# Kernel optimization log

Measured on AMD Instinct MI355X. Metric: run time of the kernel, lower is better.

## Reference

```python
import jax, jax.numpy as jnp
import numpy as np

HEADS = 6
WS = 8  # window size
EPS = 1e-12  # F.normalize default eps


def _l2norm(x):
    n = jnp.linalg.norm(x, axis=-1, keepdims=True)
    return x / jnp.maximum(n, EPS)


def setup_inputs() -> dict:
    key = jax.random.key(0)
    ks = jax.random.split(key, 5)
    B, C, H, W = 4, 192, 256, 256
    x = jax.random.normal(ks[0], (B, C, H, W), dtype=jnp.float32)
    dw_w = jax.random.normal(ks[1], (C, 1, 3, 3), dtype=jnp.float32) * 0.05
    dw_b = jax.random.normal(ks[2], (C,), dtype=jnp.float32) * 0.05
    pw_w = jax.random.normal(ks[3], (3 * C, C, 1, 1), dtype=jnp.float32) * 0.05
    pw_b = jax.random.normal(ks[4], (3 * C,), dtype=jnp.float32) * 0.05
    return {"x": x, "dw_w": dw_w, "dw_b": dw_b, "pw_w": pw_w, "pw_b": pw_b}


def reference(x, dw_w, dw_b, pw_w, pw_b):
    B, C, H, W = x.shape
    dn = ('NCHW', 'OIHW', 'NCHW')
    # SeparableConv: depthwise 3x3 (pad 1) then pointwise 1x1 -> 3C channels
    y = jax.lax.conv_general_dilated(x, dw_w, (1, 1), [(1, 1), (1, 1)],
                                     dimension_numbers=dn,
                                     feature_group_count=C) + dw_b[None, :, None, None]
    qkv = jax.lax.conv_general_dilated(y, pw_w, (1, 1), [(0, 0), (0, 0)],
                                       dimension_numbers=dn) + pw_b[None, :, None, None]
    C3 = 3 * C
    qkv = qkv.transpose(0, 2, 3, 1)  # (B, H, W, 3C)  [bchw_to_blc + view]
    # window_partition -> (B*nW, WS*WS, 3C)
    qkv = qkv.reshape(B, H // WS, WS, W // WS, WS, C3)
    qkv = qkv.transpose(0, 1, 3, 2, 4, 5).reshape(-1, WS * WS, C3)
    B_, N, _ = qkv.shape
    hd = C // HEADS
    qkv = qkv.reshape(B_, N, 3, HEADS, hd).transpose(2, 0, 3, 1, 4)
    q, k, v = qkv[0], qkv[1], qkv[2]  # each (B_, heads, N, hd)
    # cosine-similarity attention: L2-normalized q, k
    attn = jnp.einsum('bhnd,bhmd->bhnm', _l2norm(q), _l2norm(k))
    attn = jax.nn.softmax(attn, axis=-1)  # attn_drop=0.0 -> identity
    o = jnp.einsum('bhnm,bhmd->bhnd', attn, v)
    o = o.transpose(0, 2, 1, 3).reshape(B_, WS, WS, C)  # (B_, ws, ws, C)
    # window_reverse -> (B, H, W, C)
    o = o.reshape(B, H // WS, W // WS, WS, WS, C)
    o = o.transpose(0, 1, 3, 2, 4, 5).reshape(B, H, W, C)
    return o.transpose(0, 3, 1, 2)  # bhwc_to_bchw
```

## Files before the change

### kernel.cpp

```cpp
#include <hip/hip_runtime.h>
#include <hip/hip_bf16.h>

typedef float f32x4 __attribute__((ext_vector_type(4)));
typedef short bf16x8 __attribute__((ext_vector_type(8)));
typedef unsigned short u16;

#define NHEADS 6
#define CIN 192
#define HD 32
#define IMG 256
#define YS_ST 200
#define QK_ST 40
#define VT_ST 72
#define P_ST  72

__device__ __forceinline__ u16 f2bf(float f) {
    __hip_bfloat16 t = __float2bfloat16(f);
    return *reinterpret_cast<u16*>(&t);
}

template<bool CHK>
__device__ __forceinline__ void dwphase(const float* __restrict__ x,
                                        const float* __restrict__ dww,
                                        const float* __restrict__ dwb,
                                        u16 (*ys)[YS_ST],
                                        int b, int r0, int c0, int lane, int wave) {
    const int pi = lane >> 3, pj = lane & 7;
    const int py = r0 + pi, px = c0 + pj;
    for (int cb = wave * 4; cb < CIN; cb += 16) {
        float acc[4];
#pragma unroll
        for (int u = 0; u < 4; ++u) acc[u] = dwb[cb + u];
#pragma unroll
        for (int di = 0; di < 3; ++di) {
            const int yy = py + di - 1;
            const bool yok = !CHK || (unsigned)yy < (unsigned)IMG;
#pragma unroll
            for (int dj = 0; dj < 3; ++dj) {
                const int xx = px + dj - 1;
                const bool ok = !CHK || (yok && (unsigned)xx < (unsigned)IMG);
#pragma unroll
                for (int u = 0; u < 4; ++u) {
                    const float* xp = x + (((size_t)(b * CIN + cb + u)) << 16);
                    const float xv = ok ? xp[yy * IMG + xx] : 0.f;
                    acc[u] += xv * dww[(cb + u) * 9 + di * 3 + dj];
                }
            }
        }
        const unsigned lo = ((unsigned)f2bf(acc[1]) << 16) | f2bf(acc[0]);
        const unsigned hi = ((unsigned)f2bf(acc[3]) << 16) | f2bf(acc[2]);
        uint2 pk; pk.x = lo; pk.y = hi;
        *(uint2*)&ys[lane][cb] = pk;
    }
}

__global__ __launch_bounds__(256, 4)
void fused_winattn_mfma(const float* __restrict__ x,
                        const float* __restrict__ dww,
                        const float* __restrict__ dwb,
                        const float* __restrict__ pww,
                        const float* __restrict__ pwb,
                        const u16* __restrict__ wbf,
                        float* __restrict__ out) {
    __shared__ __align__(16) unsigned char smem[25600];
    u16 (*ys)[YS_ST] = (u16 (*)[YS_ST])smem;
    u16 (*qs)[QK_ST] = (u16 (*)[QK_ST])smem;
    u16 (*ks)[QK_ST] = (u16 (*)[QK_ST])(smem + 5120);
    u16 (*vt)[VT_ST] = (u16 (*)[VT_ST])(smem + 10240);
    u16 (*ps)[P_ST]  = (u16 (*)[P_ST]) (smem + 14848);

    const int bid = blockIdx.x;
    const int wb  = (bid & 7) * 512 + (bid >> 3);
    const int b   = wb >> 10;
    const int wy  = (wb >> 5) & 31;
    const int wx  = wb & 31;
    const int r0 = wy << 3, c0 = wx << 3;
    const int tid  = threadIdx.x;
    const int lane = tid & 63;
    const int wave = __builtin_amdgcn_readfirstlane(tid >> 6);
    const int l15 = lane & 15;
    const int l4  = lane >> 4;

    if ((unsigned)(wy - 1) < 30u && (unsigned)(wx - 1) < 30u)
        dwphase<false>(x, dww, dwb, ys, b, r0, c0, lane, wave);
    else
        dwphase<true>(x, dww, dwb, ys, b, r0, c0, lane, wave);
    __syncthreads();

    const int wr = wave >> 1, wc = wave & 1;
    bf16x8 afr[2][6];
#pragma unroll
    for (int rt = 0; rt < 2; ++rt) {
        const u16* ab = &ys[wr * 32 + rt * 16 + l15][l4 * 8];
#pragma unroll
        for (int kt = 0; kt < 6; ++kt)
            afr[rt][kt] = *(const bf16x8*)(ab + kt * 32);
    }
    __syncthreads();

    const int m0 = wave * 16;

    for (int h = 0; h < NHEADS; ++h) {
        const int qkbase = (wc ? CIN : 0) + h * HD;
        f32x4 acc[2][2];
#pragma unroll
        for (int ct = 0; ct < 2; ++ct) {
            const int ocrow = qkbase + ct * 16 + l15;
            const float bias = pwb[ocrow];
            acc[ct][0] = (f32x4){bias, bias, bias, bias};
            acc[ct][1] = acc[ct][0];
            bf16x8 bfr[6];
            if (wbf) {
                const u16* wp = wbf + (size_t)ocrow * CIN + l4 * 8;
#pragma unroll
                for (int kt = 0; kt < 6; ++kt) bfr[kt] = *(const bf16x8*)(wp + kt * 32);
            } else {
                const float* wp = pww + (size_t)ocrow * CIN + l4 * 8;
#pragma unroll
                for (int kt = 0; kt < 6; ++kt) {
                    union { u16 u[8]; bf16x8 v; } cv;
#pragma unroll
                    for (int i = 0; i < 8; ++i) cv.u[i] = f2bf(wp[kt * 32 + i]);
                    bfr[kt] = cv.v;
                }
            }
#pragma unroll
            for (int kt = 0; kt < 6; ++kt) {
                acc[ct][0] = __builtin_amdgcn_mfma_f32_16x16x32_bf16(afr[0][kt], bfr[kt], acc[ct][0], 0, 0, 0);
                acc[ct][1] = __builtin_amdgcn_mfma_f32_16x16x32_bf16(afr[1][kt], bfr[kt], acc[ct][1], 0, 0, 0);
            }
        }
#pragma unroll
        for (int rt = 0; rt < 2; ++rt) {
            f32x4 s;
#pragma unroll
            for (int i = 0; i < 4; ++i)
                s[i] = acc[0][rt][i] * acc[0][rt][i] + acc[1][rt][i] * acc[1][rt][i];
#pragma unroll
            for (int off = 1; off < 16; off <<= 1) {
#pragma unroll
                for (int i = 0; i < 4; ++i) s[i] += __shfl_xor(s[i], off);
            }
#pragma unroll
            for (int i = 0; i < 4; ++i) {
                const float inv = 1.f / fmaxf(sqrtf(s[i]), 1e-12f);
                acc[0][rt][i] *= inv;
                acc[1][rt][i] *= inv;
            }
            const int pxr = wr * 32 + rt * 16 + l4 * 4;
            u16 (*dst)[QK_ST] = wc ? ks : qs;
#pragma unroll
            for (int ct = 0; ct < 2; ++ct)
#pragma unroll
                for (int i = 0; i < 4; ++i)
                    dst[pxr + i][ct * 16 + l15] = f2bf(acc[ct][rt][i]);
        }
        {
            const int ocrow = 2 * CIN + h * HD + wc * 16 + l15;
            const float bias = pwb[ocrow];
            f32x4 av0 = (f32x4){bias, bias, bias, bias};
            f32x4 av1 = av0;
            bf16x8 bfr[6];
            if (wbf) {
                const u16* wp = wbf + (size_t)ocrow * CIN + l4 * 8;
#pragma unroll
                for (int kt = 0; kt < 6; ++kt) bfr[kt] = *(const bf16x8*)(wp + kt * 32);
            } else {
                const float* wp = pww + (size_t)ocrow * CIN + l4 * 8;
#pragma unroll
                for (int kt = 0; kt < 6; ++kt) {
                    union { u16 u[8]; bf16x8 v; } cv;
#pragma unroll
                    for (int i = 0; i < 8; ++i) cv.u[i] = f2bf(wp[kt * 32 + i]);
                    bfr[kt] = cv.v;
                }
            }
#pragma unroll
            for (int kt = 0; kt < 6; ++kt) {
                av0 = __builtin_amdgcn_mfma_f32_16x16x32_bf16(afr[0][kt], bfr[kt], av0, 0, 0, 0);
                av1 = __builtin_amdgcn_mfma_f32_16x16x32_bf16(afr[1][kt], bfr[kt], av1, 0, 0, 0);
            }
#pragma unroll
            for (int rt = 0; rt < 2; ++rt) {
                const f32x4 a = rt ? av1 : av0;
                const int pxr = wr * 32 + rt * 16 + l4 * 4;
                const unsigned lo = ((unsigned)f2bf(a[1]) << 16) | f2bf(a[0]);
                const unsigned hi = ((unsigned)f2bf(a[3]) << 16) | f2bf(a[2]);
                uint2 pk; pk.x = lo; pk.y = hi;
                *(uint2*)&vt[wc * 16 + l15][pxr] = pk;
            }
        }
        __syncthreads();

        const bf16x8 aq = *(const bf16x8*)&qs[m0 + l15][l4 * 8];
        f32x4 sc[4];
#pragma unroll
        for (int ct = 0; ct < 4; ++ct) {
            f32x4 z = {0.f, 0.f, 0.f, 0.f};
            const bf16x8 bk = *(const bf16x8*)&ks[ct * 16 + l15][l4 * 8];
            sc[ct] = __builtin_amdgcn_mfma_f32_16x16x32_bf16(aq, bk, z, 0, 0, 0);
        }
#pragma unroll
        for (int i = 0; i < 4; ++i) {
            float mx = fmaxf(fmaxf(sc[0][i], sc[1][i]), fmaxf(sc[2][i], sc[3][i]));
#pragma unroll
            for (int off = 1; off < 16; off <<= 1) mx = fmaxf(mx, __shfl_xor(mx, off));
            const float e0 = __expf(sc[0][i] - mx), e1 = __expf(sc[1][i] - mx);
            const float e2 = __expf(sc[2][i] - mx), e3 = __expf(sc[3][i] - mx);
            float s = e0 + e1 + e2 + e3;
#pragma unroll
            for (int off = 1; off < 16; off <<= 1) s += __shfl_xor(s, off);
            const float r = 1.f / s;
            sc[0][i] = e0 * r; sc[1][i] = e1 * r; sc[2][i] = e2 * r; sc[3][i] = e3 * r;
        }
#pragma unroll
        for (int ct = 0; ct < 4; ++ct)
#pragma unroll
            for (int i = 0; i < 4; ++i)
                ps[m0 + l4 * 4 + i][ct * 16 + l15] = f2bf(sc[ct][i]);

        const bf16x8 ap0 = *(const bf16x8*)&ps[m0 + l15][l4 * 8];
        const bf16x8 ap1 = *(const bf16x8*)&ps[m0 + l15][32 + l4 * 8];
#pragma unroll
        for (int nt = 0; nt < 2; ++nt) {
            f32x4 oa = {0.f, 0.f, 0.f, 0.f};
            const bf16x8 bv0 = *(const bf16x8*)&vt[nt * 16 + l15][l4 * 8];
            const bf16x8 bv1 = *(const bf16x8*)&vt[nt * 16 + l15][32 + l4 * 8];
            oa = __builtin_amdgcn_mfma_f32_16x16x32_bf16(ap0, bv0, oa, 0, 0, 0);
            oa = __builtin_amdgcn_mfma_f32_16x16x32_bf16(ap1, bv1, oa, 0, 0, 0);
            const int dim = h * HD + nt * 16 + l15;
            const int pxr = m0 + l4 * 4;
            const int py = r0 + (pxr >> 3), pxc = c0 + (pxr & 7);
            float* op = out + (((size_t)(b * CIN + dim)) << 16) + py * IMG + pxc;
            *(f32x4*)op = oa;
        }
        __syncthreads();
    }
}

__global__ void cvt_w(const float* __restrict__ w, u16* __restrict__ o, int n) {
    const int i = blockIdx.x * 256 + threadIdx.x;
    if (i < n) o[i] = f2bf(w[i]);
}

extern "C" void kernel_launch(void* const* d_in, const int* in_sizes, int n_in,
                              void* d_out, int out_size, void* d_ws, size_t ws_size,
                              hipStream_t stream) {
    const float* x   = (const float*)d_in[0];
    const float* dww = (const float*)d_in[1];
    const float* dwb = (const float*)d_in[2];
    const float* pww = (const float*)d_in[3];
    const float* pwb = (const float*)d_in[4];
    float* out = (float*)d_out;

    const int nw = 3 * CIN * CIN;
    u16* wbf = nullptr;
    if (ws_size >= (size_t)nw * sizeof(u16)) {
        wbf = (u16*)d_ws;
        hipLaunchKernelGGL(cvt_w, dim3(nw / 256), dim3(256), 0, stream, pww, wbf, nw);
    }
    hipLaunchKernelGGL(fused_winattn_mfma, dim3(4 * 32 * 32), dim3(256), 0, stream,
                       x, dww, dwb, pww, pwb, wbf, out);
}
```

Baseline: 371.4 us.

## Prefetch next-head pointwise weights, keep ys in LDS, transpose QK^T softmax

Each head's pointwise weight fragments and biases are now loaded into registers one head ahead, so their global-load latency overlaps with the current head's work. The ys tile moves to its own LDS region with a padded stride and its A fragments are re-read from LDS every head rather than held in registers, which also drops one barrier. The score MFMA is transposed (K as A, Q as B) so each softmax row sits within a lane and needs only two cross-lane shuffles per reduction, and probabilities are written to LDS as packed 64-bit stores. LDS use roughly doubles and the occupancy hint drops from 4 to 3 blocks, trading occupancy for fewer registers spent on ys and more latency hiding.

Measured after the change: 382.0 us. +2.8%, slower.

```diff
diff --git a/kernel.cpp b/kernel.cpp
--- a/kernel.cpp
+++ b/kernel.cpp
@@ -9,7 +9,7 @@
 #define CIN 192
 #define HD 32
 #define IMG 256
-#define YS_ST 200
+#define YS_ST 208
 #define QK_ST 40
 #define VT_ST 72
 #define P_ST  72
@@ -54,7 +54,7 @@
     }
 }
 
-__global__ __launch_bounds__(256, 4)
+__global__ __launch_bounds__(256, 3)
 void fused_winattn_mfma(const float* __restrict__ x,
                         const float* __restrict__ dww,
                         const float* __restrict__ dwb,
@@ -62,12 +62,12 @@
                         const float* __restrict__ pwb,
                         const u16* __restrict__ wbf,
                         float* __restrict__ out) {
-    __shared__ __align__(16) unsigned char smem[25600];
+    __shared__ __align__(16) unsigned char smem[50688];
     u16 (*ys)[YS_ST] = (u16 (*)[YS_ST])smem;
-    u16 (*qs)[QK_ST] = (u16 (*)[QK_ST])smem;
-    u16 (*ks)[QK_ST] = (u16 (*)[QK_ST])(smem + 5120);
-    u16 (*vt)[VT_ST] = (u16 (*)[VT_ST])(smem + 10240);
-    u16 (*ps)[P_ST]  = (u16 (*)[P_ST]) (smem + 14848);
+    u16 (*qs)[QK_ST] = (u16 (*)[QK_ST])(smem + 26624);
+    u16 (*ks)[QK_ST] = (u16 (*)[QK_ST])(smem + 31744);
+    u16 (*vt)[VT_ST] = (u16 (*)[VT_ST])(smem + 36864);
+    u16 (*ps)[P_ST]  = (u16 (*)[P_ST]) (smem + 41472);
 
     const int bid = blockIdx.x;
     const int wb  = (bid & 7) * 512 + (bid >> 3);
@@ -80,6 +80,36 @@
     const int wave = __builtin_amdgcn_readfirstlane(tid >> 6);
     const int l15 = lane & 15;
     const int l4  = lane >> 4;
+    const int wr = wave >> 1, wc = wave & 1;
+    const int m0 = wave * 16;
+
+    bf16x8 wf[3][6];
+    float biasr[3];
+    auto ldfrag = [&](int ocrow, int kt) -> bf16x8 {
+        if (wbf) {
+            return *(const bf16x8*)(wbf + (size_t)ocrow * CIN + kt * 32 + l4 * 8);
+        } else {
+            union { u16 u[8]; bf16x8 v; } cv;
+            const float* wp = pww + (size_t)ocrow * CIN + kt * 32 + l4 * 8;
+#pragma unroll
+            for (int i = 0; i < 8; ++i) cv.u[i] = f2bf(wp[i]);
+            return cv.v;
+        }
+    };
+    auto loadw = [&](int h) {
+        const int rq0 = (wc ? CIN : 0) + h * HD + l15;
+        const int rq1 = rq0 + 16;
+        const int rv  = 2 * CIN + h * HD + wc * 16 + l15;
+#pragma unroll
+        for (int kt = 0; kt < 6; ++kt) {
+            wf[0][kt] = ldfrag(rq0, kt);
+            wf[1][kt] = ldfrag(rq1, kt);
+            wf[2][kt] = ldfrag(rv, kt);
+        }
+        biasr[0] = pwb[rq0]; biasr[1] = pwb[rq1]; biasr[2] = pwb[rv];
+    };
+
+    loadw(0);
 
     if ((unsigned)(wy - 1) < 30u && (unsigned)(wx - 1) < 30u)
         dwphase<false>(x, dww, dwb, ys, b, r0, c0, lane, wave);
@@ -87,55 +117,36 @@
         dwphase<true>(x, dww, dwb, ys, b, r0, c0, lane, wave);
     __syncthreads();
 
-    const int wr = wave >> 1, wc = wave & 1;
-    bf16x8 afr[2][6];
-#pragma unroll
-    for (int rt = 0; rt < 2; ++rt) {
-        const u16* ab = &ys[wr * 32 + rt * 16 + l15][l4 * 8];
-#pragma unroll
-        for (int kt = 0; kt < 6; ++kt)
-            afr[rt][kt] = *(const bf16x8*)(ab + kt * 32);
-    }
-    __syncthreads();
-
-    const int m0 = wave * 16;
-
     for (int h = 0; h < NHEADS; ++h) {
-        const int qkbase = (wc ? CIN : 0) + h * HD;
-        f32x4 acc[2][2];
+        f32x4 accq[2][2];
+        f32x4 accv[2];
 #pragma unroll
         for (int ct = 0; ct < 2; ++ct) {
-            const int ocrow = qkbase + ct * 16 + l15;
-            const float bias = pwb[ocrow];
-            acc[ct][0] = (f32x4){bias, bias, bias, bias};
-            acc[ct][1] = acc[ct][0];
-            bf16x8 bfr[6];
-            if (wbf) {
-                const u16* wp = wbf + (size_t)ocrow * CIN + l4 * 8;
-#pragma unroll
-                for (int kt = 0; kt < 6; ++kt) bfr[kt] = *(const bf16x8*)(wp + kt * 32);
-            } else {
-                const float* wp = pww + (size_t)ocrow * CIN + l4 * 8;
-#pragma unroll
-                for (int kt = 0; kt < 6; ++kt) {
-                    union { u16 u[8]; bf16x8 v; } cv;
-#pragma unroll
-                    for (int i = 0; i < 8; ++i) cv.u[i] = f2bf(wp[kt * 32 + i]);
-                    bfr[kt] = cv.v;
-                }
-            }
-#pragma unroll
-            for (int kt = 0; kt < 6; ++kt) {
-                acc[ct][0] = __builtin_amdgcn_mfma_f32_16x16x32_bf16(afr[0][kt], bfr[kt], acc[ct][0], 0, 0, 0);
-                acc[ct][1] = __builtin_amdgcn_mfma_f32_16x16x32_bf16(afr[1][kt], bfr[kt], acc[ct][1], 0, 0, 0);
-            }
-        }
+            const float bsc = biasr[ct];
+            accq[ct][0] = (f32x4){bsc, bsc, bsc, bsc};
+            accq[ct][1] = accq[ct][0];
+        }
+        accv[0] = (f32x4){biasr[2], biasr[2], biasr[2], biasr[2]};
+        accv[1] = accv[0];
+#pragma unroll
+        for (int kt = 0; kt < 6; ++kt) {
+            const bf16x8 a0 = *(const bf16x8*)&ys[wr * 32 + l15][kt * 32 + l4 * 8];
+            const bf16x8 a1 = *(const bf16x8*)&ys[wr * 32 + 16 + l15][kt * 32 + l4 * 8];
+            accq[0][0] = __builtin_amdgcn_mfma_f32_16x16x32_bf16(a0, wf[0][kt], accq[0][0], 0, 0, 0);
+            accq[0][1] = __builtin_amdgcn_mfma_f32_16x16x32_bf16(a1, wf[0][kt], accq[0][1], 0, 0, 0);
+            accq[1][0] = __builtin_amdgcn_mfma_f32_16x16x32_bf16(a0, wf[1][kt], accq[1][0], 0, 0, 0);
+            accq[1][1] = __builtin_amdgcn_mfma_f32_16x16x32_bf16(a1, wf[1][kt], accq[1][1], 0, 0, 0);
+            accv[0]    = __builtin_amdgcn_mfma_f32_16x16x32_bf16(a0, wf[2][kt], accv[0], 0, 0, 0);
+            accv[1]    = __builtin_amdgcn_mfma_f32_16x16x32_bf16(a1, wf[2][kt], accv[1], 0, 0, 0);
+        }
+        if (h < NHEADS - 1) loadw(h + 1);
+
 #pragma unroll
         for (int rt = 0; rt < 2; ++rt) {
             f32x4 s;
 #pragma unroll
             for (int i = 0; i < 4; ++i)
-                s[i] = acc[0][rt][i] * acc[0][rt][i] + acc[1][rt][i] * acc[1][rt][i];
+                s[i] = accq[0][rt][i] * accq[0][rt][i] + accq[1][rt][i] * accq[1][rt][i];
 #pragma unroll
             for (int off = 1; off < 16; off <<= 1) {
 #pragma unroll
@@ -144,8 +155,8 @@
 #pragma unroll
             for (int i = 0; i < 4; ++i) {
                 const float inv = 1.f / fmaxf(sqrtf(s[i]), 1e-12f);
-                acc[0][rt][i] *= inv;
-                acc[1][rt][i] *= inv;
+                accq[0][rt][i] *= inv;
+                accq[1][rt][i] *= inv;
             }
             const int pxr = wr * 32 + rt * 16 + l4 * 4;
             u16 (*dst)[QK_ST] = wc ? ks : qs;
@@ -153,71 +164,52 @@
             for (int ct = 0; ct < 2; ++ct)
 #pragma unroll
                 for (int i = 0; i < 4; ++i)
-                    dst[pxr + i][ct * 16 + l15] = f2bf(acc[ct][rt][i]);
-        }
-        {
-            const int ocrow = 2 * CIN + h * HD + wc * 16 + l15;
-            const float bias = pwb[ocrow];
-            f32x4 av0 = (f32x4){bias, bias, bias, bias};
-            f32x4 av1 = av0;
-            bf16x8 bfr[6];
-            if (wbf) {
-                const u16* wp = wbf + (size_t)ocrow * CIN + l4 * 8;
-#pragma unroll
-                for (int kt = 0; kt < 6; ++kt) bfr[kt] = *(const bf16x8*)(wp + kt * 32);
-            } else {
-                const float* wp = pww + (size_t)ocrow * CIN + l4 * 8;
-#pragma unroll
-                for (int kt = 0; kt < 6; ++kt) {
-                    union { u16 u[8]; bf16x8 v; } cv;
-#pragma unroll
-                    for (int i = 0; i < 8; ++i) cv.u[i] = f2bf(wp[kt * 32 + i]);
-                    bfr[kt] = cv.v;
-                }
-            }
-#pragma unroll
-            for (int kt = 0; kt < 6; ++kt) {
-                av0 = __builtin_amdgcn_mfma_f32_16x16x32_bf16(afr[0][kt], bfr[kt], av0, 0, 0, 0);
-                av1 = __builtin_amdgcn_mfma_f32_16x16x32_bf16(afr[1][kt], bfr[kt], av1, 0, 0, 0);
-            }
-#pragma unroll
-            for (int rt = 0; rt < 2; ++rt) {
-                const f32x4 a = rt ? av1 : av0;
-                const int pxr = wr * 32 + rt * 16 + l4 * 4;
-                const unsigned lo = ((unsigned)f2bf(a[1]) << 16) | f2bf(a[0]);
-                const unsigned hi = ((unsigned)f2bf(a[3]) << 16) | f2bf(a[2]);
-                uint2 pk; pk.x = lo; pk.y = hi;
-                *(uint2*)&vt[wc * 16 + l15][pxr] = pk;
-            }
+                    dst[pxr + i][ct * 16 + l15] = f2bf(accq[ct][rt][i]);
+        }
+#pragma unroll
+        for (int rt = 0; rt < 2; ++rt) {
+            const f32x4 a = accv[rt];
+            const int pxr = wr * 32 + rt * 16 + l4 * 4;
+            const unsigned lo = ((unsigned)f2bf(a[1]) << 16) | f2bf(a[0]);
+            const unsigned hi = ((unsigned)f2bf(a[3]) << 16) | f2bf(a[2]);
+            uint2 pk; pk.x = lo; pk.y = hi;
+            *(uint2*)&vt[wc * 16 + l15][pxr] = pk;
         }
         __syncthreads();
 
         const bf16x8 aq = *(const bf16x8*)&qs[m0 + l15][l4 * 8];
-        f32x4 sc[4];
+        f32x4 st[4];
 #pragma unroll
         for (int ct = 0; ct < 4; ++ct) {
             f32x4 z = {0.f, 0.f, 0.f, 0.f};
-            const bf16x8 bk = *(const bf16x8*)&ks[ct * 16 + l15][l4 * 8];
-            sc[ct] = __builtin_amdgcn_mfma_f32_16x16x32_bf16(aq, bk, z, 0, 0, 0);
-        }
-#pragma unroll
-        for (int i = 0; i < 4; ++i) {
-            float mx = fmaxf(fmaxf(sc[0][i], sc[1][i]), fmaxf(sc[2][i], sc[3][i]));
-#pragma unroll
-            for (int off = 1; off < 16; off <<= 1) mx = fmaxf(mx, __shfl_xor(mx, off));
-            const float e0 = __expf(sc[0][i] - mx), e1 = __expf(sc[1][i] - mx);
-            const float e2 = __expf(sc[2][i] - mx), e3 = __expf(sc[3][i] - mx);
-            float s = e0 + e1 + e2 + e3;
-#pragma unroll
-            for (int off = 1; off < 16; off <<= 1) s += __shfl_xor(s, off);
-            const float r = 1.f / s;
-            sc[0][i] = e0 * r; sc[1][i] = e1 * r; sc[2][i] = e2 * r; sc[3][i] = e3 * r;
-        }
+            const bf16x8 ak = *(const bf16x8*)&ks[ct * 16 + l15][l4 * 8];
+            st[ct] = __builtin_amdgcn_mfma_f32_16x16x32_bf16(ak, aq, z, 0, 0, 0);
+        }
+        float mx = st[0][0];
 #pragma unroll
         for (int ct = 0; ct < 4; ++ct)
 #pragma unroll
-            for (int i = 0; i < 4; ++i)
-                ps[m0 + l4 * 4 + i][ct * 16 + l15] = f2bf(sc[ct][i]);
+            for (int i = 0; i < 4; ++i) mx = fmaxf(mx, st[ct][i]);
+        mx = fmaxf(mx, __shfl_xor(mx, 16));
+        mx = fmaxf(mx, __shfl_xor(mx, 32));
+        float sum = 0.f;
+#pragma unroll
+        for (int ct = 0; ct < 4; ++ct)
+#pragma unroll
+            for (int i = 0; i < 4; ++i) {
+                st[ct][i] = __expf(st[ct][i] - mx);
+                sum += st[ct][i];
+            }
+        sum += __shfl_xor(sum, 16);
+        sum += __shfl_xor(sum, 32);
+        const float rs = 1.f / sum;
+#pragma unroll
+        for (int ct = 0; ct < 4; ++ct) {
+            const unsigned lo = ((unsigned)f2bf(st[ct][1] * rs) << 16) | f2bf(st[ct][0] * rs);
+            const unsigned hi = ((unsigned)f2bf(st[ct][3] * rs) << 16) | f2bf(st[ct][2] * rs);
+            uint2 pk; pk.x = lo; pk.y = hi;
+            *(uint2*)&ps[m0 + l15][ct * 16 + l4 * 4] = pk;
+        }
 
         const bf16x8 ap0 = *(const bf16x8*)&ps[m0 + l15][l4 * 8];
         const bf16x8 ap1 = *(const bf16x8*)&ps[m0 + l15][32 + l4 * 8];
```

## Drop softmax max-subtraction, transpose score MFMA, raise occupancy bound

Applied to the files above, without the earlier changes.

Because q and k are L2-normalized, cosine scores lie in [-1,1], so the softmax max pass and its shuffle reduction are removed and exp is applied directly. The score MFMA is transposed (K as A operand), so each lane holds one query column and the row sum needs only two cross-lane shuffles. This also lets the probabilities be packed and stored to LDS as 8-byte writes. The norm now uses a hardware rsq, and launch bounds ask for 6 waves per SIMD, which may force register spills.

Result: slower. 693.3 us (+86.7%).

```diff
diff --git a/kernel.cpp b/kernel.cpp
--- a/kernel.cpp
+++ b/kernel.cpp
@@ -54,7 +54,7 @@
     }
 }
 
-__global__ __launch_bounds__(256, 4)
+__global__ __launch_bounds__(256, 6)
 void fused_winattn_mfma(const float* __restrict__ x,
                         const float* __restrict__ dww,
                         const float* __restrict__ dwb,
@@ -143,7 +143,7 @@
             }
 #pragma unroll
             for (int i = 0; i < 4; ++i) {
-                const float inv = 1.f / fmaxf(sqrtf(s[i]), 1e-12f);
+                const float inv = __builtin_amdgcn_rsqf(fmaxf(s[i], 1e-24f));
                 acc[0][rt][i] *= inv;
                 acc[1][rt][i] *= inv;
             }
@@ -193,31 +193,31 @@
         __syncthreads();
 
         const bf16x8 aq = *(const bf16x8*)&qs[m0 + l15][l4 * 8];
-        f32x4 sc[4];
+        f32x4 st[4];
 #pragma unroll
         for (int ct = 0; ct < 4; ++ct) {
             f32x4 z = {0.f, 0.f, 0.f, 0.f};
-            const bf16x8 bk = *(const bf16x8*)&ks[ct * 16 + l15][l4 * 8];
-            sc[ct] = __builtin_amdgcn_mfma_f32_16x16x32_bf16(aq, bk, z, 0, 0, 0);
-        }
-#pragma unroll
-        for (int i = 0; i < 4; ++i) {
-            float mx = fmaxf(fmaxf(sc[0][i], sc[1][i]), fmaxf(sc[2][i], sc[3][i]));
-#pragma unroll
-            for (int off = 1; off < 16; off <<= 1) mx = fmaxf(mx, __shfl_xor(mx, off));
-            const float e0 = __expf(sc[0][i] - mx), e1 = __expf(sc[1][i] - mx);
-            const float e2 = __expf(sc[2][i] - mx), e3 = __expf(sc[3][i] - mx);
-            float s = e0 + e1 + e2 + e3;
-#pragma unroll
-            for (int off = 1; off < 16; off <<= 1) s += __shfl_xor(s, off);
-            const float r = 1.f / s;
-            sc[0][i] = e0 * r; sc[1][i] = e1 * r; sc[2][i] = e2 * r; sc[3][i] = e3 * r;
-        }
+            const bf16x8 ak = *(const bf16x8*)&ks[ct * 16 + l15][l4 * 8];
+            st[ct] = __builtin_amdgcn_mfma_f32_16x16x32_bf16(ak, aq, z, 0, 0, 0);
+        }
+        float sum = 0.f;
 #pragma unroll
         for (int ct = 0; ct < 4; ++ct)
 #pragma unroll
-            for (int i = 0; i < 4; ++i)
-                ps[m0 + l4 * 4 + i][ct * 16 + l15] = f2bf(sc[ct][i]);
+            for (int i = 0; i < 4; ++i) {
+                st[ct][i] = __expf(st[ct][i]);
+                sum += st[ct][i];
+            }
+        sum += __shfl_xor(sum, 16);
+        sum += __shfl_xor(sum, 32);
+        const float rs = __builtin_amdgcn_rcpf(sum);
+#pragma unroll
+        for (int ct = 0; ct < 4; ++ct) {
+            const unsigned lo = ((unsigned)f2bf(st[ct][1] * rs) << 16) | f2bf(st[ct][0] * rs);
+            const unsigned hi = ((unsigned)f2bf(st[ct][3] * rs) << 16) | f2bf(st[ct][2] * rs);
+            uint2 pk; pk.x = lo; pk.y = hi;
+            *(uint2*)&ps[m0 + l15][ct * 16 + l4 * 4] = pk;
+        }
 
         const bf16x8 ap0 = *(const bf16x8*)&ps[m0 + l15][l4 * 8];
         const bf16x8 ap1 = *(const bf16x8*)&ps[m0 + l15][32 + l4 * 8];
```
